# Kernel optimization log

Measured on AMD Instinct MI355X. Metric: run time of the kernel, lower is better.

The kernel has to match this reference:

```python
import jax, jax.numpy as jnp
import numpy as np
from jax import lax

B, D = 512, 256
C = 10  # hidden conv channels


def setup_inputs() -> dict:
    key = jax.random.key(0)
    ks = jax.random.split(key, 9)
    x = jax.random.normal(ks[0], (B, D, D), jnp.float32)
    w1 = jax.random.normal(ks[1], (C, 1, 1, 1), jnp.float32) * 0.1   # Conv2d(1,10,1)
    b1 = jax.random.normal(ks[2], (C,), jnp.float32) * 0.01
    w2 = jax.random.normal(ks[3], (1, C, 3, 3), jnp.float32) * 0.05  # Conv2d(10,1,3,1,1)
    b2 = jax.random.normal(ks[4], (1,), jnp.float32) * 0.01
    fc1_w = jax.random.normal(ks[5], (4, D * B), jnp.float32) * (1.0 / np.sqrt(D * B))
    fc1_b = jax.random.normal(ks[6], (4,), jnp.float32) * 0.01
    fc2_w = jax.random.normal(ks[7], (2, 4), jnp.float32) * 0.5
    fc2_b = jax.random.normal(ks[8], (2,), jnp.float32) * 0.01
    return {"x": x, "w1": w1, "b1": b1, "w2": w2, "b2": b2,
            "fc1_w": fc1_w, "fc1_b": fc1_b, "fc2_w": fc2_w, "fc2_b": fc2_b}


def reference(x, w1, b1, w2, b2, fc1_w, fc1_b, fc2_w, fc2_b):
    # edge-to-edge: E[b,i,j] = row_sum(i) + col_sum(j)
    rs = x.sum(axis=-1)          # [B, D]
    cs = x.sum(axis=-2)          # [B, D]
    e = (rs[:, :, None] + cs[:, None, :])[:, None]  # [B, 1, D, D]
    # Conv2d(1, C, 1) == per-pixel scale+bias over channels
    h = jax.nn.relu(e * w1.reshape(1, C, 1, 1) + b1.reshape(1, C, 1, 1))  # [B, C, D, D]
    # convSym: lower-triangular mask each channel
    h = h * jnp.tril(jnp.ones((D, D), jnp.float32))
    # Conv2d(C, 1, 3, stride=1, pad=1)
    y = lax.conv_general_dilated(h, w2, (1, 1), 'SAME',
                                 dimension_numbers=('NCHW', 'OIHW', 'NCHW'))
    y = jax.nn.relu(y + b2.reshape(1, 1, 1, 1))[:, 0]  # [B, D, D]
    # edge-to-vertex: v[b,i] = row_sum + col_sum
    v = y.sum(axis=-1) + y.sum(axis=-2)  # [B, D]
    flat = v.reshape(-1)                  # [B*D]
    hfc = jax.nn.relu(fc1_w @ flat + fc1_b)
    return fc2_w @ hfc + fc2_b            # [2]
```

## Files before the change

kernel.cpp:

```cpp
#include <hip/hip_runtime.h>

#define DD 256
#define BB 512
#define NL 2048

#define OFF_RS   0
#define OFF_CSP  131072
#define OFF_HFC  655360
#define OFF_PAR  655368
#define OFF_TABP 655376
#define OFF_LUT  655648

typedef float v2f __attribute__((ext_vector_type(2)));

__device__ __forceinline__ v2f mk2(float a, float b) { v2f r; r.x = a; r.y = b; return r; }

__device__ __forceinline__ v2f fma2(v2f a, v2f b, v2f c) {
#if __has_builtin(__builtin_elementwise_fma)
  return __builtin_elementwise_fma(a, b, c);
#else
  return mk2(fmaf(a.x, b.x, c.x), fmaf(a.y, b.y, c.y));
#endif
}

__device__ __forceinline__ float wave_red(float v) {
#pragma unroll
  for (int off = 32; off > 0; off >>= 1) v += __shfl_down(v, off, 64);
  return v;
}

__global__ __launch_bounds__(256) void sum_kernel(const float* __restrict__ x,
                                                  const float* __restrict__ w1,
                                                  const float* __restrict__ b1,
                                                  const float* __restrict__ w2,
                                                  float* __restrict__ ws) {
  const int bq = blockIdx.x;
  const int tid = threadIdx.x;
  if (bq == 2048) {
    const int t = tid;
    float w1v[10], b1v[10], bp[10];
    int rank[10];
#pragma unroll
    for (int c = 0; c < 10; ++c) { w1v[c] = w1[c]; b1v[c] = b1[c]; bp[c] = -b1v[c] / w1v[c]; }
#pragma unroll
    for (int c = 0; c < 10; ++c) {
      int r = 0;
#pragma unroll
      for (int k = 0; k < 10; ++k)
        r += (bp[k] < bp[c] || (bp[k] == bp[c] && k < c)) ? 1 : 0;
      rank[c] = r;
    }
    float lo = bp[0], hi = bp[0];
#pragma unroll
    for (int c = 1; c < 10; ++c) { lo = fminf(lo, bp[c]); hi = fmaxf(hi, bp[c]); }
    const float step = (hi - lo) / (float)(NL - 3);
    if (t == 0) {
      ws[OFF_PAR]     = (float)(NL - 3) / (hi - lo);
      ws[OFF_PAR + 1] = 1.0f - lo * ((float)(NL - 3) / (hi - lo));
    }
    if (t < 99) {
      const int s = t / 9, tt = t % 9;
      const int dr = tt / 3, kc = tt % 3;
      float A = 0.f, Bv = 0.f;
      for (int c = 0; c < 10; ++c) {
        bool act = (w1v[c] > 0.f) ? (rank[c] < s)
                 : ((w1v[c] < 0.f) ? (rank[c] >= s) : (b1v[c] > 0.f));
        if (act) { A += w1v[c] * w2[c * 9 + tt]; Bv += b1v[c] * w2[c * 9 + tt]; }
      }
      const int base = (s * 3 + kc) * 8;
      const int posA = (dr == 2) ? 4 : dr;
      const int posB = (dr == 2) ? 5 : (2 + dr);
      ws[OFF_TABP + base + posA] = A;
      ws[OFF_TABP + base + posB] = Bv;
      ws[OFF_TABP + base + 6] = 0.f;
      ws[OFF_TABP + base + 7] = 0.f;
    }
    unsigned short* lut = (unsigned short*)(ws + OFF_LUT);
    for (int k = t; k < NL; k += 256) {
      const float xx = lo + (float)(k - 1) * step;
      int s = 0;
#pragma unroll
      for (int c = 0; c < 10; ++c) s += (bp[c] < xx) ? 1 : 0;
      lut[k] = (unsigned short)(s * 96);
    }
    return;
  }
  const int b = bq >> 2;
  const int q = bq & 3;
  const int lane = tid & 63;
  const int wv = tid >> 6;
  __shared__ float rowp[64][65];
  __shared__ float csl[4][DD];
  __shared__ float segp[4][64];
  float4 cacc = make_float4(0.f, 0.f, 0.f, 0.f);
  const float4* px = (const float4*)(x + ((size_t)b << 16) + ((size_t)(q * 64 + wv * 16) << 8));
#pragma unroll
  for (int r = 0; r < 16; ++r) {
    float4 val = px[r * 64 + lane];
    cacc.x += val.x; cacc.y += val.y; cacc.z += val.z; cacc.w += val.w;
    rowp[wv * 16 + r][lane] = (val.x + val.y) + (val.z + val.w);
  }
  ((float4*)csl[wv])[lane] = cacc;
  __syncthreads();
  {
    const int row = tid & 63, seg = tid >> 6;
    const float* rp = rowp[row] + seg * 16;
    float s = 0.f;
#pragma unroll
    for (int k = 0; k < 16; ++k) s += rp[k];
    segp[seg][row] = s;
  }
  __syncthreads();
  if (tid < 64)
    ws[OFF_RS + b * DD + q * 64 + tid] =
        (segp[0][tid] + segp[1][tid]) + (segp[2][tid] + segp[3][tid]);
  ws[OFF_CSP + bq * DD + tid] =
      (csl[0][tid] + csl[1][tid]) + (csl[2][tid] + csl[3][tid]);
  if (bq == 0 && tid < 4) ws[OFF_HFC + tid] = 0.f;
}

__global__ __launch_bounds__(1024, 8) void conv_kernel(const float* __restrict__ b2p,
                                                       const float* __restrict__ fc1w,
                                                       float* __restrict__ ws) {
  const int b = blockIdx.x;
  const int tid = threadIdx.x;
  const int w = tid >> 6;
  const int lane = tid & 63;

  int wb, r0, r1;
  switch (w) {
    case 0:  wb = 0; r0 = 0;   r1 = 43;  break;
    case 1:  wb = 0; r0 = 43;  r1 = 86;  break;
    case 2:  wb = 0; r0 = 86;  r1 = 129; break;
    case 3:  wb = 0; r0 = 129; r1 = 172; break;
    case 4:  wb = 0; r0 = 172; r1 = 214; break;
    case 5:  wb = 0; r0 = 214; r1 = 256; break;
    case 6:  wb = 1; r0 = 62;  r1 = 101; break;
    case 7:  wb = 1; r0 = 101; r1 = 140; break;
    case 8:  wb = 1; r0 = 140; r1 = 179; break;
    case 9:  wb = 1; r0 = 179; r1 = 218; break;
    case 10: wb = 1; r0 = 218; r1 = 256; break;
    case 11: wb = 2; r0 = 126; r1 = 170; break;
    case 12: wb = 2; r0 = 170; r1 = 213; break;
    case 13: wb = 2; r0 = 213; r1 = 256; break;
    case 14: wb = 3; r0 = 190; r1 = 223; break;
    default: wb = 3; r0 = 223; r1 = 256; break;
  }
  const int jmin = wb * 64;
  const int j = jmin + lane;

  __shared__ __align__(16) float tabP[264];
  __shared__ float rs_s[DD];
  __shared__ float cs_s[DD];
  __shared__ __align__(16) float wkA[DD][4];
  __shared__ unsigned short lut_s[NL];
  __shared__ float segsum_s[4][4];
  __shared__ float red_s[64];

  ((unsigned int*)lut_s)[tid] = ((const unsigned int*)(ws + OFF_LUT))[tid];
  if (tid < 256) {
    rs_s[tid] = ws[OFF_RS + b * DD + tid];
  } else if (tid < 512) {
    const int t = tid - 256;
    const float* csp = ws + OFF_CSP + (b * 4) * DD + t;
    cs_s[t] = (csp[0] + csp[DD]) + (csp[2 * DD] + csp[3 * DD]);
  } else if (tid < 768) {
    const int r = tid - 512;
#pragma unroll
    for (int k = 0; k < 4; ++k) wkA[r][k] = fc1w[k * (BB * DD) + b * DD + r];
  } else {
    const int u = tid - 768;
    if (u < 256) tabP[u] = ws[OFF_TABP + u];
  }
  if (tid < 8) tabP[256 + tid] = ws[OFF_TABP + 256 + tid];
  __syncthreads();
  if (tid < 16) {
    const int ss = tid >> 2, k = tid & 3;
    float s = 0.f;
#pragma unroll
    for (int r = 0; r < 64; ++r) s += wkA[ss * 64 + r][k];
    segsum_s[ss][k] = s;
  }
  __syncthreads();

  const float inv_step = ws[OFF_PAR];
  const float bias = ws[OFF_PAR + 1];
  const float b2v = b2p[0];
  const float yb = fmaxf(b2v, 0.f);
  const float fxmax = (float)(NL - 1);

  float csr[3], vf[3];
  csr[0] = (j >= 1) ? cs_s[j - 1] : 0.f;
  csr[1] = cs_s[j];
  csr[2] = (j < DD - 1) ? cs_s[j + 1] : 0.f;
  vf[0] = (j >= 1) ? 1.f : 0.f;
  vf[1] = 1.f;
  vf[2] = (j < DD - 1) ? 1.f : 0.f;
  v2f vf2[3];
#pragma unroll
  for (int kc = 0; kc < 3; ++kc) vf2[kc] = mk2(vf[kc], vf[kc]);

  const int dlim = jmin + 63;
  const int iend = (r1 == DD) ? DD - 1 : r1;

  float P = 0.f, Q = 0.f;
  float vcol = 0.f;
  v2f a01 = mk2(0.f, 0.f);
  v2f a23 = mk2(0.f, 0.f);

#define TAP_CORE(KC, E, M2, MS)                                              \
  {                                                                          \
    float fx = fmaf((E), inv_step, bias);                                    \
    fx = fminf(fmaxf(fx, 0.f), fxmax);                                       \
    const int off = (int)lut_s[(int)fx];                                     \
    const char* tp = (const char*)tabP + (off + (KC) * 32);                  \
    const float4 ab = *(const float4*)tp;                   \
    const float2 ab2 = *(const float2*)(tp + 16);                 \
    v2f tv = fma2(mk2(ab.x, ab.y), mk2((E), (E)), mk2(ab.z, ab.w));          \
    R01 = fma2((M2), tv, R01);                                               \
    R2 = fmaf((MS), fmaf(ab2.x, (E), ab2.y), R2);                            \
  }

  if (r0 >= dlim) {
    for (int i = r0 - 1; i <= r0; ++i) {
      const float rsv = rs_s[i];
      v2f R01 = mk2(0.f, 0.f); float R2 = 0.f;
#pragma unroll
      for (int kc = 0; kc < 3; ++kc) {
        const float e = rsv + csr[kc];
        const float m = ((j - 1 + kc) <= i) ? vf[kc] : 0.f;
        TAP_CORE(kc, e, mk2(m, m), m)
      }
      (void)R2;
      P = Q + R01.y; Q = R01.x;
    }
    for (int i = r0 + 1; i <= iend; ++i) {
      const float rsv = rs_s[i];
      v2f R01 = mk2(0.f, 0.f); float R2 = 0.f;
#pragma unroll
      for (int kc = 0; kc < 3; ++kc) {
        const float e = rsv + csr[kc];
        TAP_CORE(kc, e, vf2[kc], vf[kc])
      }
      const float yd = fmaxf(P + R2 + b2v, 0.f) - yb;
      vcol += yd;
      const float4 wkv = *(const float4*)wkA[i - 1];
      a01 = fma2(mk2(yd, yd), mk2(wkv.x, wkv.y), a01);
      a23 = fma2(mk2(yd, yd), mk2(wkv.z, wkv.w), a23);
      P = Q + R01.y; Q = R01.x;
    }
  } else {
    const int ibeg = (r0 == 0) ? 0 : r0 - 1;
    const int ffrom = r0 + 1;
    const int gend = (iend < dlim) ? iend : dlim;
    for (int i = ibeg; i <= gend; ++i) {
      const float rsv = rs_s[i];
      v2f R01 = mk2(0.f, 0.f); float R2 = 0.f;
      if (j - 1 <= i) {
#pragma unroll
        for (int kc = 0; kc < 3; ++kc) {
          const float e = rsv + csr[kc];
          const float m = ((j - 1 + kc) <= i) ? vf[kc] : 0.f;
          TAP_CORE(kc, e, mk2(m, m), m)
        }
      }
      if (i >= ffrom) {
        const float yd = fmaxf(P + R2 + b2v, 0.f) - yb;
        vcol += yd;
        const float4 wkv = *(const float4*)wkA[i - 1];
        a01 = fma2(mk2(yd, yd), mk2(wkv.x, wkv.y), a01);
        a23 = fma2(mk2(yd, yd), mk2(wkv.z, wkv.w), a23);
      }
      P = Q + R01.y; Q = R01.x;
    }
    for (int i = dlim + 1; i <= iend; ++i) {
      const float rsv = rs_s[i];
      v2f R01 = mk2(0.f, 0.f); float R2 = 0.f;
#pragma unroll
      for (int kc = 0; kc < 3; ++kc) {
        const float e = rsv + csr[kc];
        TAP_CORE(kc, e, vf2[kc], vf[kc])
      }
      const float yd = fmaxf(P + R2 + b2v, 0.f) - yb;
      vcol += yd;
      const float4 wkv = *(const float4*)wkA[i - 1];
      a01 = fma2(mk2(yd, yd), mk2(wkv.x, wkv.y), a01);
      a23 = fma2(mk2(yd, yd), mk2(wkv.z, wkv.w), a23);
      P = Q + R01.y; Q = R01.x;
    }
  }
  if (r1 == DD) {
    const float yd = fmaxf(P + b2v, 0.f) - yb;
    vcol += yd;
    const float4 wkv = *(const float4*)wkA[DD - 1];
    a01 = fma2(mk2(yd, yd), mk2(wkv.x, wkv.y), a01);
    a23 = fma2(mk2(yd, yd), mk2(wkv.z, wkv.w), a23);
  }

  const float4 wkj = *(const float4*)wkA[j];
  a01 = fma2(mk2(vcol, vcol), mk2(wkj.x, wkj.y), a01);
  a23 = fma2(mk2(vcol, vcol), mk2(wkj.z, wkj.w), a23);

  float acc0 = wave_red(a01.x), acc1 = wave_red(a01.y);
  float acc2 = wave_red(a23.x), acc3 = wave_red(a23.y);
  if (lane == 0) {
    red_s[w * 4 + 0] = acc0; red_s[w * 4 + 1] = acc1;
    red_s[w * 4 + 2] = acc2; red_s[w * 4 + 3] = acc3;
  }
  __syncthreads();
  if (tid < 4) {
    float s = 0.f;
#pragma unroll
    for (int wv = 0; wv < 16; ++wv) s += red_s[wv * 4 + tid];
    const float wt = (segsum_s[0][tid] + segsum_s[1][tid]) +
                     (segsum_s[2][tid] + segsum_s[3][tid]);
    s = fmaf(512.f * yb, wt, s);
    atomicAdd(&ws[OFF_HFC + tid], s);
  }
#undef TAP_CORE
}

__global__ void fc_kernel(const float* __restrict__ fc1b, const float* __restrict__ fc2w,
                          const float* __restrict__ fc2b, const float* __restrict__ ws,
                          float* __restrict__ out) {
  if (threadIdx.x == 0 && blockIdx.x == 0) {
    float o0 = fc2b[0], o1 = fc2b[1];
#pragma unroll
    for (int k = 0; k < 4; ++k) {
      float h = fmaxf(ws[OFF_HFC + k] + fc1b[k], 0.f);
      o0 += fc2w[k] * h;
      o1 += fc2w[4 + k] * h;
    }
    out[0] = o0; out[1] = o1;
  }
}

extern "C" void kernel_launch(void* const* d_in, const int* in_sizes, int n_in,
                              void* d_out, int out_size, void* d_ws, size_t ws_size,
                              hipStream_t stream) {
  const float* x    = (const float*)d_in[0];
  const float* w1   = (const float*)d_in[1];
  const float* b1   = (const float*)d_in[2];
  const float* w2   = (const float*)d_in[3];
  const float* b2   = (const float*)d_in[4];
  const float* fc1w = (const float*)d_in[5];
  const float* fc1b = (const float*)d_in[6];
  const float* fc2w = (const float*)d_in[7];
  const float* fc2b = (const float*)d_in[8];
  float* out = (float*)d_out;
  float* ws  = (float*)d_ws;

  hipLaunchKernelGGL(sum_kernel,  dim3(2049), dim3(256), 0, stream, x, w1, b1, w2, ws);
  hipLaunchKernelGGL(conv_kernel, dim3(512), dim3(1024), 0, stream, b2, fc1w, ws);
  hipLaunchKernelGGL(fc_kernel,   dim3(1), dim3(64), 0, stream, fc1b, fc2w, fc2b, ws, out);
}
```

Baseline: 239.7 us.

## Replace LUT piecewise lookup with hoisted linear baseline plus rare breakpoint path

Drops the 2048-entry quantized lookup table. The conv taps are now evaluated as a per-column precomputed affine baseline (the all-inactive-regime coefficients folded with the column sums) plus a correction for inputs above the highest ReLU breakpoint. A wave-uniform slow path counts breakpoints exactly only when some lane falls inside the breakpoint range. This removes the per-tap LDS table lookups and gathers for most iterations. It also splits each batch's conv across two 512-thread blocks instead of one 1024-thread block, which adds a second atomic per batch and more divergence when waves take the slow path.

```diff
diff --git a/kernel.cpp b/kernel.cpp
--- a/kernel.cpp
+++ b/kernel.cpp
@@ -2,14 +2,13 @@
 
 #define DD 256
 #define BB 512
-#define NL 2048
 
 #define OFF_RS   0
 #define OFF_CSP  131072
 #define OFF_HFC  655360
 #define OFF_PAR  655368
-#define OFF_TABP 655376
-#define OFF_LUT  655648
+#define OFF_TABP 655384
+#define OFF_TABO 655648
 
 typedef float v2f __attribute__((ext_vector_type(2)));
 
@@ -27,6 +26,10 @@
 #pragma unroll
   for (int off = 32; off > 0; off >>= 1) v += __shfl_down(v, off, 64);
   return v;
+}
+
+__device__ __forceinline__ float rfl(float v) {
+  return __uint_as_float(__builtin_amdgcn_readfirstlane(__float_as_uint(v)));
 }
 
 __global__ __launch_bounds__(256) void sum_kernel(const float* __restrict__ x,
@@ -53,11 +56,8 @@
     float lo = bp[0], hi = bp[0];
 #pragma unroll
     for (int c = 1; c < 10; ++c) { lo = fminf(lo, bp[c]); hi = fmaxf(hi, bp[c]); }
-    const float step = (hi - lo) / (float)(NL - 3);
-    if (t == 0) {
-      ws[OFF_PAR]     = (float)(NL - 3) / (hi - lo);
-      ws[OFF_PAR + 1] = 1.0f - lo * ((float)(NL - 3) / (hi - lo));
-    }
+    if (t == 0) { ws[OFF_PAR] = lo; ws[OFF_PAR + 1] = hi; }
+    if (t >= 16 && t < 26) ws[OFF_PAR + 2 + (t - 16)] = bp[t - 16];
     if (t < 99) {
       const int s = t / 9, tt = t % 9;
       const int dr = tt / 3, kc = tt % 3;
@@ -67,21 +67,20 @@
                  : ((w1v[c] < 0.f) ? (rank[c] >= s) : (b1v[c] > 0.f));
         if (act) { A += w1v[c] * w2[c * 9 + tt]; Bv += b1v[c] * w2[c * 9 + tt]; }
       }
+      float A0 = 0.f, B0 = 0.f;
+      for (int c = 0; c < 10; ++c) {
+        bool act0 = (w1v[c] < 0.f) || (w1v[c] == 0.f && b1v[c] > 0.f);
+        if (act0) { A0 += w1v[c] * w2[c * 9 + tt]; B0 += b1v[c] * w2[c * 9 + tt]; }
+      }
       const int base = (s * 3 + kc) * 8;
       const int posA = (dr == 2) ? 4 : dr;
       const int posB = (dr == 2) ? 5 : (2 + dr);
-      ws[OFF_TABP + base + posA] = A;
-      ws[OFF_TABP + base + posB] = Bv;
-      ws[OFF_TABP + base + 6] = 0.f;
-      ws[OFF_TABP + base + 7] = 0.f;
-    }
-    unsigned short* lut = (unsigned short*)(ws + OFF_LUT);
-    for (int k = t; k < NL; k += 256) {
-      const float xx = lo + (float)(k - 1) * step;
-      int s = 0;
-#pragma unroll
-      for (int c = 0; c < 10; ++c) s += (bp[c] < xx) ? 1 : 0;
-      lut[k] = (unsigned short)(s * 96);
+      ws[OFF_TABO + base + posA] = A;
+      ws[OFF_TABO + base + posB] = Bv;
+      ws[OFF_TABP + base + posA] = A - A0;
+      ws[OFF_TABP + base + posB] = Bv - B0;
+      ws[OFF_TABO + base + 6] = 0.f; ws[OFF_TABO + base + 7] = 0.f;
+      ws[OFF_TABP + base + 6] = 0.f; ws[OFF_TABP + base + 7] = 0.f;
     }
     return;
   }
@@ -119,16 +118,18 @@
   if (bq == 0 && tid < 4) ws[OFF_HFC + tid] = 0.f;
 }
 
-__global__ __launch_bounds__(1024, 8) void conv_kernel(const float* __restrict__ b2p,
-                                                       const float* __restrict__ fc1w,
-                                                       float* __restrict__ ws) {
-  const int b = blockIdx.x;
+__global__ __launch_bounds__(512, 6) void conv_kernel(const float* __restrict__ b2p,
+                                                      const float* __restrict__ fc1w,
+                                                      float* __restrict__ ws) {
+  const int b = blockIdx.x >> 1;
+  const int h = blockIdx.x & 1;
   const int tid = threadIdx.x;
   const int w = tid >> 6;
   const int lane = tid & 63;
+  const int run = (h << 3) | w;
 
   int wb, r0, r1;
-  switch (w) {
+  switch (run) {
     case 0:  wb = 0; r0 = 0;   r1 = 43;  break;
     case 1:  wb = 0; r0 = 43;  r1 = 86;  break;
     case 2:  wb = 0; r0 = 86;  r1 = 129; break;
@@ -148,31 +149,41 @@
   }
   const int jmin = wb * 64;
   const int j = jmin + lane;
-
-  __shared__ __align__(16) float tabP[264];
+  const int dlim = jmin + 63;
+
+  __shared__ __align__(16) float tabD_s[264];
+  __shared__ __align__(16) float tabO_s[264];
   __shared__ float rs_s[DD];
   __shared__ float cs_s[DD];
   __shared__ __align__(16) float wkA[DD][4];
-  __shared__ unsigned short lut_s[NL];
   __shared__ float segsum_s[4][4];
-  __shared__ float red_s[64];
-
-  ((unsigned int*)lut_s)[tid] = ((const unsigned int*)(ws + OFF_LUT))[tid];
+  __shared__ float red_s[32];
+
+  const float* par = ws + OFF_PAR;
+  const float lo_s = rfl(par[0]);
+  const float hi_s = rfl(par[1]);
+  float bp_r[10];
+#pragma unroll
+  for (int c = 0; c < 10; ++c) bp_r[c] = rfl(par[2 + c]);
+  float dH[3][6];
+  {
+    const float* dhp = ws + OFF_TABP + 240;
+#pragma unroll
+    for (int kc = 0; kc < 3; ++kc)
+#pragma unroll
+      for (int m = 0; m < 6; ++m) dH[kc][m] = rfl(dhp[kc * 8 + m]);
+  }
+
   if (tid < 256) {
     rs_s[tid] = ws[OFF_RS + b * DD + tid];
-  } else if (tid < 512) {
+#pragma unroll
+    for (int k = 0; k < 4; ++k) wkA[tid][k] = fc1w[k * (BB * DD) + b * DD + tid];
+  } else {
     const int t = tid - 256;
     const float* csp = ws + OFF_CSP + (b * 4) * DD + t;
     cs_s[t] = (csp[0] + csp[DD]) + (csp[2 * DD] + csp[3 * DD]);
-  } else if (tid < 768) {
-    const int r = tid - 512;
-#pragma unroll
-    for (int k = 0; k < 4; ++k) wkA[r][k] = fc1w[k * (BB * DD) + b * DD + r];
-  } else {
-    const int u = tid - 768;
-    if (u < 256) tabP[u] = ws[OFF_TABP + u];
-  }
-  if (tid < 8) tabP[256 + tid] = ws[OFF_TABP + 256 + tid];
+  }
+  if (tid < 264) { tabD_s[tid] = ws[OFF_TABP + tid]; tabO_s[tid] = ws[OFF_TABO + tid]; }
   __syncthreads();
   if (tid < 16) {
     const int ss = tid >> 2, k = tid & 3;
@@ -183,11 +194,8 @@
   }
   __syncthreads();
 
-  const float inv_step = ws[OFF_PAR];
-  const float bias = ws[OFF_PAR + 1];
   const float b2v = b2p[0];
   const float yb = fmaxf(b2v, 0.f);
-  const float fxmax = (float)(NL - 1);
 
   float csr[3], vf[3];
   csr[0] = (j >= 1) ? cs_s[j - 1] : 0.f;
@@ -200,53 +208,98 @@
 #pragma unroll
   for (int kc = 0; kc < 3; ++kc) vf2[kc] = mk2(vf[kc], vf[kc]);
 
-  const int dlim = jmin + 63;
+  v2f al01 = mk2(0.f, 0.f), be01 = mk2(0.f, 0.f);
+  float al2 = 0.f, be2 = 0.f;
+  {
+    const float* lop = ws + OFF_TABO;
+#pragma unroll
+    for (int kc = 0; kc < 3; ++kc) {
+      const float A0 = rfl(lop[kc * 8 + 0]), A1 = rfl(lop[kc * 8 + 1]);
+      const float B0 = rfl(lop[kc * 8 + 2]), B1 = rfl(lop[kc * 8 + 3]);
+      const float A2 = rfl(lop[kc * 8 + 4]), B2 = rfl(lop[kc * 8 + 5]);
+      const v2f a = mk2(A0, A1);
+      al01 = fma2(vf2[kc], a, al01);
+      be01 = fma2(vf2[kc], fma2(a, mk2(csr[kc], csr[kc]), mk2(B0, B1)), be01);
+      al2 = fmaf(vf[kc], A2, al2);
+      be2 = fmaf(vf[kc], fmaf(A2, csr[kc], B2), be2);
+    }
+  }
+
   const int iend = (r1 == DD) ? DD - 1 : r1;
-
   float P = 0.f, Q = 0.f;
   float vcol = 0.f;
   v2f a01 = mk2(0.f, 0.f);
   v2f a23 = mk2(0.f, 0.f);
 
-#define TAP_CORE(KC, E, M2, MS)                                              \
-  {                                                                          \
-    float fx = fmaf((E), inv_step, bias);                                    \
-    fx = fminf(fmaxf(fx, 0.f), fxmax);                                       \
-    const int off = (int)lut_s[(int)fx];                                     \
-    const char* tp = (const char*)tabP + (off + (KC) * 32);                  \
-    const float4 ab = *(const float4*)tp;                   \
-    const float2 ab2 = *(const float2*)(tp + 16);                 \
-    v2f tv = fma2(mk2(ab.x, ab.y), mk2((E), (E)), mk2(ab.z, ab.w));          \
-    R01 = fma2((M2), tv, R01);                                               \
-    R2 = fmaf((MS), fmaf(ab2.x, (E), ab2.y), R2);                            \
-  }
-
-  if (r0 >= dlim) {
-    for (int i = r0 - 1; i <= r0; ++i) {
-      const float rsv = rs_s[i];
-      v2f R01 = mk2(0.f, 0.f); float R2 = 0.f;
+  auto fast_eval = [&](float rsv, v2f& R01, float& R2) {
+    R01 = fma2(al01, mk2(rsv, rsv), be01);
+    R2 = fmaf(al2, rsv, be2);
+    int ia = 0;
+#pragma unroll
+    for (int kc = 0; kc < 3; ++kc) {
+      const float e = rsv + csr[kc];
+      const bool hib = e > hi_s;
+      const v2f tv = fma2(mk2(e, e), mk2(dH[kc][0], dH[kc][1]), mk2(dH[kc][2], dH[kc][3]));
+      const v2f mh2 = hib ? vf2[kc] : mk2(0.f, 0.f);
+      R01 = fma2(mh2, tv, R01);
+      const float t2 = fmaf(e, dH[kc][4], dH[kc][5]);
+      R2 = fmaf(hib ? vf[kc] : 0.f, t2, R2);
+      ia |= (!hib && (e > lo_s)) ? 1 : 0;
+    }
+    if (__any(ia)) {
 #pragma unroll
       for (int kc = 0; kc < 3; ++kc) {
         const float e = rsv + csr[kc];
-        const float m = ((j - 1 + kc) <= i) ? vf[kc] : 0.f;
-        TAP_CORE(kc, e, mk2(m, m), m)
+        if ((e > lo_s) && (e <= hi_s)) {
+          int s = 0;
+#pragma unroll
+          for (int c = 0; c < 10; ++c) s += (bp_r[c] < e) ? 1 : 0;
+          const char* tp = (const char*)tabD_s + s * 96 + kc * 32;
+          const float4 ab = *(const float4*)tp;
+          const float2 ab2 = *(const float2*)(tp + 16);
+          const v2f tv = fma2(mk2(ab.x, ab.y), mk2(e, e), mk2(ab.z, ab.w));
+          R01 = fma2(vf2[kc], tv, R01);
+          R2 = fmaf(vf[kc], fmaf(ab2.x, e, ab2.y), R2);
+        }
       }
-      (void)R2;
+    }
+  };
+
+  auto guard_eval = [&](float rsv, int i, v2f& R01, float& R2) {
+#pragma unroll
+    for (int kc = 0; kc < 3; ++kc) {
+      const float e = rsv + csr[kc];
+      const float m = ((j - 1 + kc) <= i) ? vf[kc] : 0.f;
+      int s = 0;
+#pragma unroll
+      for (int c = 0; c < 10; ++c) s += (bp_r[c] < e) ? 1 : 0;
+      const char* tp = (const char*)tabO_s + s * 96 + kc * 32;
+      const float4 ab = *(const float4*)tp;
+      const float2 ab2 = *(const float2*)(tp + 16);
+      const v2f tv = fma2(mk2(ab.x, ab.y), mk2(e, e), mk2(ab.z, ab.w));
+      R01 = fma2(mk2(m, m), tv, R01);
+      R2 = fmaf(m, fmaf(ab2.x, e, ab2.y), R2);
+    }
+  };
+
+  auto finalize = [&](int i, float R2v) {
+    const float yd = fmaxf(P + R2v + b2v, 0.f) - yb;
+    vcol += yd;
+    const float4 wkv = *(const float4*)wkA[i - 1];
+    a01 = fma2(mk2(yd, yd), mk2(wkv.x, wkv.y), a01);
+    a23 = fma2(mk2(yd, yd), mk2(wkv.z, wkv.w), a23);
+  };
+
+  if (r0 >= dlim + 2) {
+    for (int i = r0 - 1; i <= r0; ++i) {
+      v2f R01; float R2;
+      fast_eval(rs_s[i], R01, R2);
       P = Q + R01.y; Q = R01.x;
     }
     for (int i = r0 + 1; i <= iend; ++i) {
-      const float rsv = rs_s[i];
-      v2f R01 = mk2(0.f, 0.f); float R2 = 0.f;
-#pragma unroll
-      for (int kc = 0; kc < 3; ++kc) {
-        const float e = rsv + csr[kc];
-        TAP_CORE(kc, e, vf2[kc], vf[kc])
-      }
-      const float yd = fmaxf(P + R2 + b2v, 0.f) - yb;
-      vcol += yd;
-      const float4 wkv = *(const float4*)wkA[i - 1];
-      a01 = fma2(mk2(yd, yd), mk2(wkv.x, wkv.y), a01);
-      a23 = fma2(mk2(yd, yd), mk2(wkv.z, wkv.w), a23);
+      v2f R01; float R2;
+      fast_eval(rs_s[i], R01, R2);
+      finalize(i, R2);
       P = Q + R01.y; Q = R01.x;
     }
   } else {
@@ -254,38 +307,15 @@
     const int ffrom = r0 + 1;
     const int gend = (iend < dlim) ? iend : dlim;
     for (int i = ibeg; i <= gend; ++i) {
-      const float rsv = rs_s[i];
       v2f R01 = mk2(0.f, 0.f); float R2 = 0.f;
-      if (j - 1 <= i) {
-#pragma unroll
-        for (int kc = 0; kc < 3; ++kc) {
-          const float e = rsv + csr[kc];
-          const float m = ((j - 1 + kc) <= i) ? vf[kc] : 0.f;
-          TAP_CORE(kc, e, mk2(m, m), m)
-        }
-      }
-      if (i >= ffrom) {
-        const float yd = fmaxf(P + R2 + b2v, 0.f) - yb;
-        vcol += yd;
-        const float4 wkv = *(const float4*)wkA[i - 1];
-        a01 = fma2(mk2(yd, yd), mk2(wkv.x, wkv.y), a01);
-        a23 = fma2(mk2(yd, yd), mk2(wkv.z, wkv.w), a23);
-      }
+      if (j - 1 <= i) guard_eval(rs_s[i], i, R01, R2);
+      if (i >= ffrom) finalize(i, R2);
       P = Q + R01.y; Q = R01.x;
     }
     for (int i = dlim + 1; i <= iend; ++i) {
-      const float rsv = rs_s[i];
-      v2f R01 = mk2(0.f, 0.f); float R2 = 0.f;
-#pragma unroll
-      for (int kc = 0; kc < 3; ++kc) {
-        const float e = rsv + csr[kc];
-        TAP_CORE(kc, e, vf2[kc], vf[kc])
-      }
-      const float yd = fmaxf(P + R2 + b2v, 0.f) - yb;
-      vcol += yd;
-      const float4 wkv = *(const float4*)wkA[i - 1];
-      a01 = fma2(mk2(yd, yd), mk2(wkv.x, wkv.y), a01);
-      a23 = fma2(mk2(yd, yd), mk2(wkv.z, wkv.w), a23);
+      v2f R01; float R2;
+      fast_eval(rs_s[i], R01, R2);
+      finalize(i, R2);
       P = Q + R01.y; Q = R01.x;
     }
   }
@@ -311,13 +341,12 @@
   if (tid < 4) {
     float s = 0.f;
 #pragma unroll
-    for (int wv = 0; wv < 16; ++wv) s += red_s[wv * 4 + tid];
+    for (int wv = 0; wv < 8; ++wv) s += red_s[wv * 4 + tid];
     const float wt = (segsum_s[0][tid] + segsum_s[1][tid]) +
                      (segsum_s[2][tid] + segsum_s[3][tid]);
-    s = fmaf(512.f * yb, wt, s);
+    s = fmaf(256.f * yb, wt, s);
     atomicAdd(&ws[OFF_HFC + tid], s);
   }
-#undef TAP_CORE
 }
 
 __global__ void fc_kernel(const float* __restrict__ fc1b, const float* __restrict__ fc2w,
@@ -351,6 +380,6 @@
   float* ws  = (float*)d_ws;
 
   hipLaunchKernelGGL(sum_kernel,  dim3(2049), dim3(256), 0, stream, x, w1, b1, w2, ws);
-  hipLaunchKernelGGL(conv_kernel, dim3(512), dim3(1024), 0, stream, b2, fc1w, ws);
+  hipLaunchKernelGGL(conv_kernel, dim3(1024), dim3(512), 0, stream, b2, fc1w, ws);
   hipLaunchKernelGGL(fc_kernel,   dim3(1), dim3(64), 0, stream, fc1b, fc2w, fc2b, ws, out);
 }
```

Measured after the change: 263.6 us. 1.1x slower.
